# Optimization experiments

Hardware: AMD Instinct MI355X
Metric: run time of the kernel (lower is better)

Reference implementation:

```python
import jax, jax.numpy as jnp
import numpy as np

C_M, C_H, C_Z = 256, 32, 128
LN_EPS = 1e-5
MASK_EPS = 1e-8


def setup_inputs() -> dict:
    key = jax.random.key(0)
    ks = jax.random.split(key, 8)
    B, N, L = 1, 128, 256
    m = jax.random.normal(ks[0], (B, N, L, C_M), dtype=jnp.float32)
    msa_mask = jnp.ones((B, N, L), dtype=jnp.float32)
    # parameters
    ln_gamma = jnp.ones((C_M,), dtype=jnp.float32)
    ln_beta = jnp.zeros((C_M,), dtype=jnp.float32)
    sa = 1.0 / np.sqrt(C_M)
    Wa = jax.random.uniform(ks[1], (C_M, C_H), jnp.float32, -sa, sa)
    ba = jax.random.uniform(ks[2], (C_H,), jnp.float32, -sa, sa)
    Wb = jax.random.uniform(ks[3], (C_M, C_H), jnp.float32, -sa, sa)
    bb = jax.random.uniform(ks[4], (C_H,), jnp.float32, -sa, sa)
    so = 1.0 / np.sqrt(C_H * C_H)
    Wo = jax.random.uniform(ks[5], (C_H * C_H, C_Z), jnp.float32, -so, so)
    bo = jax.random.uniform(ks[6], (C_Z,), jnp.float32, -so, so)
    return {"m": m, "msa_mask": msa_mask, "ln_gamma": ln_gamma, "ln_beta": ln_beta,
            "Wa": Wa, "ba": ba, "Wb": Wb, "bb": bb, "Wo": Wo, "bo": bo}


def reference(m, msa_mask, ln_gamma, ln_beta, Wa, ba, Wb, bb, Wo, bo):
    B, N, L, _ = m.shape
    # LayerNorm over c_m
    mu = jnp.mean(m, axis=-1, keepdims=True)
    var = jnp.mean(jnp.square(m - mu), axis=-1, keepdims=True)
    x = (m - mu) * jax.lax.rsqrt(var + LN_EPS) * ln_gamma + ln_beta
    a = x @ Wa + ba                       # [B,N,L,c_h]
    b = x @ Wb + bb                       # [B,N,L,c_h]
    mk = msa_mask[..., None]
    a = a * mk
    b = b * mk
    # outer product mean over MSA depth: [B,L,L,c_h,c_h]
    outer = jnp.einsum('bnic,bnjd->bijcd', a, b)
    pair_mask = jnp.einsum('bni,bnj->bij', msa_mask, msa_mask)
    outer = outer / (pair_mask[..., None, None] + MASK_EPS)
    outer = outer.reshape(B, L, L, -1)    # [B,L,L,c_h*c_h]
    z_update = outer @ Wo + bo            # [B,L,L,c_z]
    return z_update
```

## Files before the change

### kernel.cpp

```cpp
#include <hip/hip_runtime.h>
#include <hip/hip_bf16.h>


typedef __attribute__((ext_vector_type(8))) short bf8_t;
typedef __attribute__((ext_vector_type(4))) float f32x4;

__device__ __forceinline__ unsigned short f2bf(float f) {
    unsigned int u = __float_as_uint(f);
    u += 0x7fffu + ((u >> 16) & 1u);
    return (unsigned short)(u >> 16);
}
__device__ __forceinline__ unsigned int pack2(float a, float b) {
    return (unsigned int)f2bf(a) | ((unsigned int)f2bf(b) << 16);
}

__global__ __launch_bounds__(256) void k_prep(const float* __restrict__ Wa,
                                              const float* __restrict__ Wb,
                                              unsigned short* __restrict__ WTb) {
    int u = blockIdx.x * 256 + threadIdx.x;
    int h = u >> 8, c = u & 255;
    float v = (h < 32) ? Wa[c * 32 + h] : Wb[c * 32 + (h - 32)];
    WTb[u] = f2bf(v);
}

__global__ __launch_bounds__(256) void k_ln_proj(
    const float* __restrict__ gm, const float* __restrict__ gmask,
    const float* __restrict__ gamma, const float* __restrict__ beta,
    const unsigned short* __restrict__ WTb,
    const float* __restrict__ ba, const float* __restrict__ bb,
    const float* __restrict__ Wo,
    unsigned short* __restrict__ aT, unsigned short* __restrict__ bT,
    unsigned short* __restrict__ W2, float* __restrict__ pmr)
{
    const int tid = threadIdx.x;
    const int tail = (int)blockIdx.x - 2048;
    if (tail >= 0) {
        if (tail < 512) {
            int u = tail * 256 + tid;
            int k = u >> 7, z = u & 127;
            int c = k >> 5, d = k & 31;
            int kp = d * 32 + c;
            int dst = (((z >> 4) * 32 + (kp >> 5)) * 16 + (z & 15)) * 32
                      + ((kp >> 3) & 3) * 8 + (kp & 7);
            W2[dst] = f2bf(Wo[u]);
        } else {
            int u = (tail - 512) * 256 + tid;
            int i = u >> 8, j = u & 255;
            float s = 0.f;
            #pragma unroll 8
            for (int n = 0; n < 128; n++)
                s += gmask[n * 256 + i] * gmask[n * 256 + j];
            pmr[u] = 1.f / (s + 1e-8f);
        }
        return;
    }

    __shared__ __align__(16) unsigned short xlb[16 * 256];
    __shared__ float vl[16 * 64];
    const int lane = tid & 63, w = tid >> 6;
    const int l = blockIdx.x & 255, n0 = ((int)blockIdx.x >> 8) << 4;

    const float4 g4  = ((const float4*)gamma)[lane];
    const float4 be4 = ((const float4*)beta)[lane];

    #pragma unroll
    for (int j = 0; j < 4; j++) {
        int row = w * 4 + j;
        int n = n0 + row;
        float4 v = ((const float4*)(gm + ((size_t)n * 256 + l) * 256))[lane];
        float s = v.x + v.y + v.z + v.w;
        float q = v.x * v.x + v.y * v.y + v.z * v.z + v.w * v.w;
        #pragma unroll
        for (int off = 1; off < 64; off <<= 1) {
            s += __shfl_xor(s, off);
            q += __shfl_xor(q, off);
        }
        float mean = s * (1.f / 256.f);
        float var = fmaxf(q * (1.f / 256.f) - mean * mean, 0.f);
        float rstd = rsqrtf(var + 1e-5f);
        float x0 = (v.x - mean) * rstd * g4.x + be4.x;
        float x1 = (v.y - mean) * rstd * g4.y + be4.y;
        float x2 = (v.z - mean) * rstd * g4.z + be4.z;
        float x3 = (v.w - mean) * rstd * g4.w + be4.w;
        int c8s = lane ^ ((row & 7) << 1);
        *(uint2*)((char*)xlb + row * 512 + (c8s << 3)) =
            make_uint2(pack2(x0, x1), pack2(x2, x3));
    }
    __syncthreads();

    const int kg = lane >> 4, r16 = lane & 15;
    const int h = w * 16 + r16;
    f32x4 acc = {0.f, 0.f, 0.f, 0.f};
    #pragma unroll
    for (int ks = 0; ks < 8; ks++) {
        int c8 = ks * 8 + kg * 2;
        bf8_t af = *(const bf8_t*)((char*)xlb + r16 * 512 +
                                   ((c8 ^ ((r16 & 7) << 1)) << 3));
        bf8_t wf = *(const bf8_t*)(WTb + (size_t)h * 256 + ks * 32 + kg * 8);
        acc = __builtin_amdgcn_mfma_f32_16x16x32_bf16(af, wf, acc, 0, 0, 0);
    }
    float bias = (h < 32) ? ba[h] : bb[h - 32];
    #pragma unroll
    for (int r = 0; r < 4; r++) {
        int nrow = kg * 4 + r;
        float mk = gmask[(size_t)(n0 + nrow) * 256 + l];
        vl[nrow * 64 + h] = (acc[r] + bias) * mk;
    }
    __syncthreads();

    if (tid < 128) {
        int row = tid >> 1, half = tid & 1;
        int hh = row & 31;
        unsigned short* dst = (row < 32) ? aT : bT;
        unsigned int pk[4];
        #pragma unroll
        for (int jj = 0; jj < 4; jj++)
            pk[jj] = pack2(vl[(half * 8 + 2 * jj) * 64 + row],
                           vl[(half * 8 + 2 * jj + 1) * 64 + row]);
        *(uint4*)(dst + ((size_t)l * 32 + hh) * 128 + n0 + half * 8) =
            make_uint4(pk[0], pk[1], pk[2], pk[3]);
    }
}

__global__ __launch_bounds__(512) void k_outer(
    const unsigned short* __restrict__ aT, const unsigned short* __restrict__ bT,
    const unsigned short* __restrict__ W2, const float* __restrict__ pmr,
    const float* __restrict__ bo, float* __restrict__ out)
{
    __shared__ __align__(16) char smem[32768];
    const int tid = threadIdx.x, lane = tid & 63, w = tid >> 6;
    const int wr = w >> 2, wc = w & 3;
    const int tj = blockIdx.x & 63, ti = blockIdx.x >> 6;
    const int kg = lane >> 4, r16 = lane & 15;

    f32x4 acc[4][2];
    #pragma unroll
    for (int mt = 0; mt < 4; mt++)
        #pragma unroll
        for (int nt = 0; nt < 2; nt++)
            acc[mt][nt] = (f32x4){0.f, 0.f, 0.f, 0.f};

    const uint4* gA = (const uint4*)(aT + (size_t)ti * 16384);
    const uint4* gB = (const uint4*)(bT + (size_t)tj * 16384);

    #pragma unroll
    for (int half = 0; half < 2; half++) {
        #pragma unroll
        for (int k = 0; k < 2; k++) {
            int g = k * 512 + tid;
            int row = g >> 3, ch = g & 7;
            int dsto = row * 128 + ((ch ^ (row & 7)) << 4);
            *(uint4*)(smem + dsto)         = gA[row * 16 + half * 8 + ch];
            *(uint4*)(smem + 16384 + dsto) = gB[row * 16 + half * 8 + ch];
        }
        __syncthreads();
        #pragma unroll
        for (int ks2 = 0; ks2 < 2; ks2++) {
            bf8_t af[4], bfr[2];
            int ch = ks2 * 4 + kg;
            #pragma unroll
            for (int mt = 0; mt < 4; mt++) {
                int mm = wr * 64 + mt * 16 + r16;
                af[mt] = *(const bf8_t*)(smem + mm * 128 + ((ch ^ (mm & 7)) << 4));
            }
            #pragma unroll
            for (int nt = 0; nt < 2; nt++) {
                int nn = wc * 32 + nt * 16 + r16;
                bfr[nt] = *(const bf8_t*)(smem + 16384 + nn * 128 + ((ch ^ (nn & 7)) << 4));
            }
            #pragma unroll
            for (int mt = 0; mt < 4; mt++)
                #pragma unroll
                for (int nt = 0; nt < 2; nt++)
                    acc[mt][nt] = __builtin_amdgcn_mfma_f32_16x16x32_bf16(
                        af[mt], bfr[nt], acc[mt][nt], 0, 0, 0);
        }
        __syncthreads();
    }

    unsigned short* O2b = (unsigned short*)smem;
    #pragma unroll
    for (int mt = 0; mt < 4; mt++) {
        int mmb = wr * 64 + mt * 16 + kg * 4;
        #pragma unroll
        for (int nt = 0; nt < 2; nt++) {
            int nn = wc * 32 + nt * 16 + r16;
            int p  = ((mmb >> 5) << 2) | (nn >> 5);
            int k2 = ((nn & 31) << 5) | (mmb & 31);
            int c2 = k2 >> 3;
            int pc = c2 ^ ((c2 >> 3) & 7) ^ (p & 7);
            *(uint2*)(O2b + p * 1024 + pc * 8 + (k2 & 7)) =
                make_uint2(pack2(acc[mt][nt][0], acc[mt][nt][1]),
                           pack2(acc[mt][nt][2], acc[mt][nt][3]));
        }
    }
    __syncthreads();

    f32x4 acc2 = {0.f, 0.f, 0.f, 0.f};
    const unsigned short* O2r = O2b + r16 * 1024;
    const int psw = r16 & 7;
    const unsigned short* wz = W2 + (size_t)w * 16384 + r16 * 32 + kg * 8;
    #pragma unroll 8
    for (int s = 0; s < 32; s++) {
        int c2 = s * 4 + kg;
        int pc = c2 ^ ((c2 >> 3) & 7) ^ psw;
        bf8_t av = *(const bf8_t*)(O2r + pc * 8);
        bf8_t wf = *(const bf8_t*)(wz + s * 512);
        acc2 = __builtin_amdgcn_mfma_f32_16x16x32_bf16(av, wf, acc2, 0, 0, 0);
    }

    const int i0 = ti * 4, j0 = tj * 4;
    const int z = w * 16 + r16;
    const float boz = bo[z];
    #pragma unroll
    for (int r = 0; r < 4; r++) {
        int p = kg * 4 + r;
        int i = i0 + (p >> 2), j = j0 + (p & 3);
        float recip = pmr[i * 256 + j];
        out[((size_t)(i * 256 + j)) * 128 + z] = acc2[r] * recip + boz;
    }
}

extern "C" void kernel_launch(void* const* d_in, const int* in_sizes, int n_in,
                              void* d_out, int out_size, void* d_ws, size_t ws_size,
                              hipStream_t stream)
{
    const float* m    = (const float*)d_in[0];
    const float* mask = (const float*)d_in[1];
    const float* gam  = (const float*)d_in[2];
    const float* bet  = (const float*)d_in[3];
    const float* Wa   = (const float*)d_in[4];
    const float* ba   = (const float*)d_in[5];
    const float* Wb   = (const float*)d_in[6];
    const float* bb   = (const float*)d_in[7];
    const float* Wo   = (const float*)d_in[8];
    const float* bo   = (const float*)d_in[9];
    float* out = (float*)d_out;

    unsigned short* aT  = (unsigned short*)d_ws;
    unsigned short* bT  = aT + 8192 * 128;
    unsigned short* W2  = bT + 8192 * 128;
    unsigned short* WTb = W2 + 128 * 1024;
    float* pmr = (float*)(WTb + 64 * 256);

    k_prep   <<<  64, 256, 0, stream>>>(Wa, Wb, WTb);
    k_ln_proj<<<2816, 256, 0, stream>>>(m, mask, gam, bet, WTb, ba, bb, Wo,
                                        aT, bT, W2, pmr);
    k_outer  <<<4096, 512, 0, stream>>>(aT, bT, W2, pmr, bo, out);
}
```

Measured before the change: 185.1 us.

## Load outer-product fragments directly from global and move Wo/mask prep into k_prep

The outer-product kernel no longer stages the aT/bT tiles through swizzled LDS with two barrier pairs. Each wave now reads its MFMA fragments straight from global memory (L2/L1-cached, since many blocks share tiles), which drops the staging stores and syncs. Separately, the Wo reordering and pair-mask reciprocal work moves out of the tail of k_ln_proj into k_prep, so the LN kernel launches a uniform grid. The trade-off is that fragment loads are now 16-byte strided global reads that depend on cache hits instead of reused LDS data.

```diff
diff --git a/kernel.cpp b/kernel.cpp
--- a/kernel.cpp
+++ b/kernel.cpp
@@ -14,13 +14,36 @@
     return (unsigned int)f2bf(a) | ((unsigned int)f2bf(b) << 16);
 }
 
-__global__ __launch_bounds__(256) void k_prep(const float* __restrict__ Wa,
-                                              const float* __restrict__ Wb,
-                                              unsigned short* __restrict__ WTb) {
-    int u = blockIdx.x * 256 + threadIdx.x;
-    int h = u >> 8, c = u & 255;
-    float v = (h < 32) ? Wa[c * 32 + h] : Wb[c * 32 + (h - 32)];
-    WTb[u] = f2bf(v);
+__global__ __launch_bounds__(256) void k_prep(
+    const float* __restrict__ Wa, const float* __restrict__ Wb,
+    const float* __restrict__ Wo, const float* __restrict__ gmask,
+    unsigned short* __restrict__ WTb, unsigned short* __restrict__ W2,
+    float* __restrict__ pmr)
+{
+    const int tid = threadIdx.x;
+    int b = blockIdx.x;
+    if (b < 64) {
+        int u = b * 256 + tid;
+        int h = u >> 8, c = u & 255;
+        float v = (h < 32) ? Wa[c * 32 + h] : Wb[c * 32 + (h - 32)];
+        WTb[u] = f2bf(v);
+    } else if (b < 576) {
+        int u = (b - 64) * 256 + tid;
+        int k = u >> 7, z = u & 127;
+        int c = k >> 5, d = k & 31;
+        int kp = d * 32 + c;
+        int dst = (((z >> 4) * 32 + (kp >> 5)) * 16 + (z & 15)) * 32
+                  + ((kp >> 3) & 3) * 8 + (kp & 7);
+        W2[dst] = f2bf(Wo[u]);
+    } else {
+        int u = (b - 576) * 256 + tid;
+        int i = u >> 8, j = u & 255;
+        float s = 0.f;
+        #pragma unroll 8
+        for (int n = 0; n < 128; n++)
+            s += gmask[n * 256 + i] * gmask[n * 256 + j];
+        pmr[u] = 1.f / (s + 1e-8f);
+    }
 }
 
 __global__ __launch_bounds__(256) void k_ln_proj(
@@ -28,35 +51,11 @@
     const float* __restrict__ gamma, const float* __restrict__ beta,
     const unsigned short* __restrict__ WTb,
     const float* __restrict__ ba, const float* __restrict__ bb,
-    const float* __restrict__ Wo,
-    unsigned short* __restrict__ aT, unsigned short* __restrict__ bT,
-    unsigned short* __restrict__ W2, float* __restrict__ pmr)
-{
-    const int tid = threadIdx.x;
-    const int tail = (int)blockIdx.x - 2048;
-    if (tail >= 0) {
-        if (tail < 512) {
-            int u = tail * 256 + tid;
-            int k = u >> 7, z = u & 127;
-            int c = k >> 5, d = k & 31;
-            int kp = d * 32 + c;
-            int dst = (((z >> 4) * 32 + (kp >> 5)) * 16 + (z & 15)) * 32
-                      + ((kp >> 3) & 3) * 8 + (kp & 7);
-            W2[dst] = f2bf(Wo[u]);
-        } else {
-            int u = (tail - 512) * 256 + tid;
-            int i = u >> 8, j = u & 255;
-            float s = 0.f;
-            #pragma unroll 8
-            for (int n = 0; n < 128; n++)
-                s += gmask[n * 256 + i] * gmask[n * 256 + j];
-            pmr[u] = 1.f / (s + 1e-8f);
-        }
-        return;
-    }
-
+    unsigned short* __restrict__ aT, unsigned short* __restrict__ bT)
+{
     __shared__ __align__(16) unsigned short xlb[16 * 256];
     __shared__ float vl[16 * 64];
+    const int tid = threadIdx.x;
     const int lane = tid & 63, w = tid >> 6;
     const int l = blockIdx.x & 255, n0 = ((int)blockIdx.x >> 8) << 4;
 
@@ -140,42 +139,23 @@
         for (int nt = 0; nt < 2; nt++)
             acc[mt][nt] = (f32x4){0.f, 0.f, 0.f, 0.f};
 
-    const uint4* gA = (const uint4*)(aT + (size_t)ti * 16384);
-    const uint4* gB = (const uint4*)(bT + (size_t)tj * 16384);
-
-    #pragma unroll
-    for (int half = 0; half < 2; half++) {
-        #pragma unroll
-        for (int k = 0; k < 2; k++) {
-            int g = k * 512 + tid;
-            int row = g >> 3, ch = g & 7;
-            int dsto = row * 128 + ((ch ^ (row & 7)) << 4);
-            *(uint4*)(smem + dsto)         = gA[row * 16 + half * 8 + ch];
-            *(uint4*)(smem + 16384 + dsto) = gB[row * 16 + half * 8 + ch];
-        }
-        __syncthreads();
-        #pragma unroll
-        for (int ks2 = 0; ks2 < 2; ks2++) {
-            bf8_t af[4], bfr[2];
-            int ch = ks2 * 4 + kg;
+    const unsigned short* Abase = aT + ((size_t)(ti * 128 + wr * 64 + r16)) * 128 + kg * 8;
+    const unsigned short* Bbase = bT + ((size_t)(tj * 128 + wc * 32 + r16)) * 128 + kg * 8;
+    #pragma unroll
+    for (int ks = 0; ks < 4; ks++) {
+        bf8_t af[4], bfr[2];
+        #pragma unroll
+        for (int mt = 0; mt < 4; mt++)
+            af[mt] = *(const bf8_t*)(Abase + mt * 16 * 128 + ks * 32);
+        #pragma unroll
+        for (int nt = 0; nt < 2; nt++)
+            bfr[nt] = *(const bf8_t*)(Bbase + nt * 16 * 128 + ks * 32);
+        #pragma unroll
+        for (int mt = 0; mt < 4; mt++)
             #pragma unroll
-            for (int mt = 0; mt < 4; mt++) {
-                int mm = wr * 64 + mt * 16 + r16;
-                af[mt] = *(const bf8_t*)(smem + mm * 128 + ((ch ^ (mm & 7)) << 4));
-            }
-            #pragma unroll
-            for (int nt = 0; nt < 2; nt++) {
-                int nn = wc * 32 + nt * 16 + r16;
-                bfr[nt] = *(const bf8_t*)(smem + 16384 + nn * 128 + ((ch ^ (nn & 7)) << 4));
-            }
-            #pragma unroll
-            for (int mt = 0; mt < 4; mt++)
-                #pragma unroll
-                for (int nt = 0; nt < 2; nt++)
-                    acc[mt][nt] = __builtin_amdgcn_mfma_f32_16x16x32_bf16(
-                        af[mt], bfr[nt], acc[mt][nt], 0, 0, 0);
-        }
-        __syncthreads();
+            for (int nt = 0; nt < 2; nt++)
+                acc[mt][nt] = __builtin_amdgcn_mfma_f32_16x16x32_bf16(
+                    af[mt], bfr[nt], acc[mt][nt], 0, 0, 0);
     }
 
     unsigned short* O2b = (unsigned short*)smem;
@@ -243,8 +223,7 @@
     unsigned short* WTb = W2 + 128 * 1024;
     float* pmr = (float*)(WTb + 64 * 256);
 
-    k_prep   <<<  64, 256, 0, stream>>>(Wa, Wb, WTb);
-    k_ln_proj<<<2816, 256, 0, stream>>>(m, mask, gam, bet, WTb, ba, bb, Wo,
-                                        aT, bT, W2, pmr);
+    k_prep   <<< 832, 256, 0, stream>>>(Wa, Wb, Wo, mask, WTb, W2, pmr);
+    k_ln_proj<<<2048, 256, 0, stream>>>(m, mask, gam, bet, WTb, ba, bb, aT, bT);
     k_outer  <<<4096, 512, 0, stream>>>(aT, bT, W2, pmr, bo, out);
 }
```

New measurement: 255.5 us. 1.38x slower.
